# Kernel tuning notes

Measured on AMD Instinct MI355X. Metric: run time of the kernel, lower is better.

The kernel has to match this reference:

```python
import jax, jax.numpy as jnp
import numpy as np

N = 11  # moving-average window (layer __init__ arg)


def setup_inputs() -> dict:
    key = jax.random.key(0)
    x = jax.random.normal(key, (8, 16384, 256), dtype=jnp.float32)  # [batch, time, channels]
    return {"x": x}


def reference(x):
    # np.convolve(x[i,:,j], ones(N)/N, mode='same') along the time axis for every
    # (batch, channel) pair. The uniform kernel is symmetric, so convolution ==
    # correlation; 'same' takes the centered slice starting at (N-1)//2 of the
    # full convolution. Implemented as a prefix-sum box filter (O(1) per element).
    B, T, C = x.shape
    s = (N - 1) // 2            # np.convolve 'same' center offset
    lo, hi = N - 1 - s, s       # zero padding implied by 'same'
    xp = jnp.pad(x, ((0, 0), (lo, hi), (0, 0)))          # [B, T+N-1, C]
    c = jnp.cumsum(xp, axis=1)
    c = jnp.pad(c, ((0, 0), (1, 0), (0, 0)))             # prefix zero -> [B, T+N, C]
    out = (c[:, N:, :] - c[:, :T, :]) * (1.0 / N)        # windowed sums / N
    return out
```

## Files before the change

### kernel.cpp

```cpp
#include <hip/hip_runtime.h>

namespace {

constexpr int T   = 16384;
constexpr int B   = 8;
constexpr int C4  = 64;
constexpr int SUB = 8;
constexpr int NROWS = SUB + 10;
constexpr int WAVES_PER_BLOCK = 4;
constexpr int BLOCK_T = SUB * WAVES_PER_BLOCK;

typedef float vfloat4 __attribute__((ext_vector_type(4)));

template <bool GUARD>
__device__ __forceinline__ float4 ldx(const float4* __restrict__ xb, int tt) {
    if (GUARD) {
        if (tt < 0 || tt >= T) return float4{0.f, 0.f, 0.f, 0.f};
    }
    return xb[(size_t)tt * C4];
}

__device__ __forceinline__ void stnt(float4* p, float4 v) {
    vfloat4 nv = {v.x, v.y, v.z, v.w};
    __builtin_nontemporal_store(nv, (vfloat4*)p);
}

template <bool GUARD>
__device__ __forceinline__ void run_chunk(const float4* __restrict__ xb,
                                          float4* __restrict__ ob, int t0) {
    constexpr float INV = 1.0f / 11.0f;

    float4 r[NROWS];
    #pragma unroll
    for (int i = 0; i < NROWS; ++i) {
        r[i] = ldx<GUARD>(xb, t0 - 5 + i);
    }
    __builtin_amdgcn_sched_barrier(0);

    float4 s = {0.f, 0.f, 0.f, 0.f};
    #pragma unroll
    for (int i = 0; i < 11; ++i) {
        s.x += r[i].x; s.y += r[i].y; s.z += r[i].z; s.w += r[i].w;
    }
    float4 o;
    o.x = s.x * INV; o.y = s.y * INV; o.z = s.z * INV; o.w = s.w * INV;
    stnt(&ob[(size_t)t0 * C4], o);

    #pragma unroll
    for (int i = 1; i < SUB; ++i) {
        const float4 a = r[i + 10];
        const float4 d = r[i - 1];
        s.x += a.x - d.x; s.y += a.y - d.y; s.z += a.z - d.z; s.w += a.w - d.w;
        o.x = s.x * INV; o.y = s.y * INV; o.z = s.z * INV; o.w = s.w * INV;
        stnt(&ob[(size_t)(t0 + i) * C4], o);
    }
}

__global__ __launch_bounds__(256, 2) void runavg_kernel(const float4* __restrict__ x,
                                                        float4* __restrict__ out) {
    const int lane = threadIdx.x & 63;
    const int wid  = threadIdx.x >> 6;
    const int chunks_per_batch = T / BLOCK_T;
    const int b  = blockIdx.x / chunks_per_batch;
    const int t0 = (blockIdx.x % chunks_per_batch) * BLOCK_T + wid * SUB;

    const float4* __restrict__ xb = x   + (size_t)b * T * C4 + lane;
    float4* __restrict__       ob = out + (size_t)b * T * C4 + lane;

    if (t0 >= 5 && t0 + SUB + 5 <= T) {
        run_chunk<false>(xb, ob, t0);
    } else {
        run_chunk<true>(xb, ob, t0);
    }
}

}

extern "C" void kernel_launch(void* const* d_in, const int* in_sizes, int n_in,
                              void* d_out, int out_size, void* d_ws, size_t ws_size,
                              hipStream_t stream) {
    const float4* x = (const float4*)d_in[0];
    float4* out = (float4*)d_out;
    const int grid = B * (T / BLOCK_T);
    runavg_kernel<<<grid, 256, 0, stream>>>(x, out);
}
```

Before: 48.97 us.

## Stage block time tile in LDS via direct global-to-LDS loads

```diff
diff --git a/kernel.cpp b/kernel.cpp
--- a/kernel.cpp
+++ b/kernel.cpp
@@ -6,36 +6,70 @@
 constexpr int B   = 8;
 constexpr int C4  = 64;
 constexpr int SUB = 8;
-constexpr int NROWS = SUB + 10;
-constexpr int WAVES_PER_BLOCK = 4;
-constexpr int BLOCK_T = SUB * WAVES_PER_BLOCK;
+constexpr int WAVES = 4;
+constexpr int BLOCK_T = SUB * WAVES;
+constexpr int ROWS = BLOCK_T + 10;
+constexpr int CHUNKS = T / BLOCK_T;
+constexpr int ROW_B = C4 * 16;
 
 typedef float vfloat4 __attribute__((ext_vector_type(4)));
-
-template <bool GUARD>
-__device__ __forceinline__ float4 ldx(const float4* __restrict__ xb, int tt) {
-    if (GUARD) {
-        if (tt < 0 || tt >= T) return float4{0.f, 0.f, 0.f, 0.f};
-    }
-    return xb[(size_t)tt * C4];
-}
+typedef __attribute__((address_space(3))) void lds_void;
+typedef const __attribute__((address_space(1))) void gbl_void;
 
 __device__ __forceinline__ void stnt(float4* p, float4 v) {
     vfloat4 nv = {v.x, v.y, v.z, v.w};
     __builtin_nontemporal_store(nv, (vfloat4*)p);
 }
 
-template <bool GUARD>
-__device__ __forceinline__ void run_chunk(const float4* __restrict__ xb,
-                                          float4* __restrict__ ob, int t0) {
+__global__ __launch_bounds__(256) void runavg_kernel(const float4* __restrict__ x,
+                                                     float4* __restrict__ out) {
+    __shared__ float4 lds[ROWS * C4];
+
+    const int tid  = threadIdx.x;
+    const int lane = tid & 63;
+    const int wid  = tid >> 6;
+    const int b    = blockIdx.x / CHUNKS;
+    const int t0b  = (blockIdx.x % CHUNKS) * BLOCK_T;
+
+    const bool first = (t0b == 0);
+    const bool last  = (t0b + BLOCK_T == T);
+    const bool guard = first || last;
+
+    const float* xf = (const float*)x;
+    #pragma unroll
+    for (int it = 0; it < 11; ++it) {
+        const int r = it * 4 + wid;
+        if (r < ROWS) {
+            const int t = t0b - 5 + r;
+            if (!guard || ((unsigned)t < (unsigned)T)) {
+                const float* gp = xf + ((size_t)b * T + t) * 256 + lane * 4;
+                __builtin_amdgcn_global_load_lds((gbl_void*)gp,
+                                                 (lds_void*)((char*)lds + r * ROW_B),
+                                                 16, 0, 0);
+            }
+        }
+    }
+
+    if (guard) {
+        const float4 z = make_float4(0.f, 0.f, 0.f, 0.f);
+        for (int u = tid; u < 5 * C4; u += 256) {
+            const int rr = u >> 6, cc = u & 63;
+            if (first) lds[rr * C4 + cc] = z;
+            if (last)  lds[(ROWS - 5 + rr) * C4 + cc] = z;
+        }
+    }
+    __syncthreads();
+
     constexpr float INV = 1.0f / 11.0f;
-
-    float4 r[NROWS];
+    const int t0 = t0b + wid * SUB;
+    float4 r[SUB + 10];
     #pragma unroll
-    for (int i = 0; i < NROWS; ++i) {
-        r[i] = ldx<GUARD>(xb, t0 - 5 + i);
+    for (int i = 0; i < SUB + 10; ++i) {
+        r[i] = lds[(wid * SUB + i) * C4 + lane];
     }
     __builtin_amdgcn_sched_barrier(0);
+
+    float4* ob = out + ((size_t)b * T + t0) * C4 + lane;
 
     float4 s = {0.f, 0.f, 0.f, 0.f};
     #pragma unroll
@@ -44,7 +78,7 @@
     }
     float4 o;
     o.x = s.x * INV; o.y = s.y * INV; o.z = s.z * INV; o.w = s.w * INV;
-    stnt(&ob[(size_t)t0 * C4], o);
+    stnt(ob, o);
 
     #pragma unroll
     for (int i = 1; i < SUB; ++i) {
@@ -52,25 +86,7 @@
         const float4 d = r[i - 1];
         s.x += a.x - d.x; s.y += a.y - d.y; s.z += a.z - d.z; s.w += a.w - d.w;
         o.x = s.x * INV; o.y = s.y * INV; o.z = s.z * INV; o.w = s.w * INV;
-        stnt(&ob[(size_t)(t0 + i) * C4], o);
-    }
-}
-
-__global__ __launch_bounds__(256, 2) void runavg_kernel(const float4* __restrict__ x,
-                                                        float4* __restrict__ out) {
-    const int lane = threadIdx.x & 63;
-    const int wid  = threadIdx.x >> 6;
-    const int chunks_per_batch = T / BLOCK_T;
-    const int b  = blockIdx.x / chunks_per_batch;
-    const int t0 = (blockIdx.x % chunks_per_batch) * BLOCK_T + wid * SUB;
-
-    const float4* __restrict__ xb = x   + (size_t)b * T * C4 + lane;
-    float4* __restrict__       ob = out + (size_t)b * T * C4 + lane;
-
-    if (t0 >= 5 && t0 + SUB + 5 <= T) {
-        run_chunk<false>(xb, ob, t0);
-    } else {
-        run_chunk<true>(xb, ob, t0);
+        stnt(ob + (size_t)i * C4, o);
     }
 }
 
@@ -81,6 +97,6 @@
                               hipStream_t stream) {
     const float4* x = (const float4*)d_in[0];
     float4* out = (float4*)d_out;
-    const int grid = B * (T / BLOCK_T);
+    const int grid = B * CHUNKS;
     runavg_kernel<<<grid, 256, 0, stream>>>(x, out);
 }
```

Result: no change. 49.51 us (+1.1%).
